# Kernel tuning notes

Measured on AMD Instinct MI355X. Metric: run time of the kernel, lower is better.

The kernel has to match this reference:

```python
import jax, jax.numpy as jnp
import numpy as np

N = 100_000   # nodes
E = 1_600_000 # edges
F = 32        # input features
G = 512       # graphs in batch
EPS = 1e-5    # batchnorm eps


def setup_inputs() -> dict:
    key = jax.random.key(0)
    ks = jax.random.split(key, 24)
    d = {
        "x": jax.random.normal(ks[0], (N, F), jnp.float32),
        "edge_index": jax.random.randint(ks[1], (2, E), 0, N),
        "batch": jnp.sort(jax.random.randint(ks[2], (N,), 0, G)),
        "Wl1": jax.random.normal(ks[3], (30, F), jnp.float32) * 0.1,
        "bl1": jax.random.normal(ks[4], (30,), jnp.float32) * 0.1,
        "Wr1": jax.random.normal(ks[5], (30, F), jnp.float32) * 0.1,
        "Wl2": jax.random.normal(ks[6], (30, 30), jnp.float32) * 0.1,
        "bl2": jax.random.normal(ks[7], (30,), jnp.float32) * 0.1,
        "Wr2": jax.random.normal(ks[8], (30, 30), jnp.float32) * 0.1,
        "g1": jax.random.uniform(ks[9], (30,), jnp.float32) + 0.5,
        "b1": jax.random.normal(ks[10], (30,), jnp.float32) * 0.1,
        "m1": jax.random.normal(ks[11], (30,), jnp.float32) * 0.1,
        "v1": jax.random.uniform(ks[12], (30,), jnp.float32) + 0.5,
        "g2": jax.random.uniform(ks[13], (30,), jnp.float32) + 0.5,
        "b2": jax.random.normal(ks[14], (30,), jnp.float32) * 0.1,
        "m2": jax.random.normal(ks[15], (30,), jnp.float32) * 0.1,
        "v2": jax.random.uniform(ks[16], (30,), jnp.float32) + 0.5,
        "W1": jax.random.normal(ks[17], (10, 60), jnp.float32) * 0.1,
        "bb1": jax.random.normal(ks[18], (10,), jnp.float32) * 0.1,
        "W2": jax.random.normal(ks[19], (1, 10), jnp.float32) * 0.1,
        "bb2": jax.random.normal(ks[20], (1,), jnp.float32) * 0.1,
    }
    return d


def reference(x, edge_index, batch, Wl1, bl1, Wr1, Wl2, bl2, Wr2,
              g1, b1, m1, v1, g2, b2, m2, v2, W1, bb1, W2, bb2):
    src, dst = edge_index[0], edge_index[1]

    def sage(h, Wl, bl, Wr):
        # mean aggregation of source features into targets (PyG SAGEConv default)
        s = jax.ops.segment_sum(h[src], dst, num_segments=N)
        cnt = jax.ops.segment_sum(jnp.ones((E,), h.dtype), dst, num_segments=N)
        agg = s / jnp.maximum(cnt, 1.0)[:, None]
        return agg @ Wl.T + bl + h @ Wr.T

    def bn(h, g, b, m, v):  # BatchNorm1d, eval mode (running stats)
        return (h - m) * jax.lax.rsqrt(v + EPS) * g + b

    h = bn(jax.nn.relu(sage(x, Wl1, bl1, Wr1)), g1, b1, m1, v1)
    h = bn(jax.nn.relu(sage(h, Wl2, bl2, Wr2)), g2, b2, m2, v2)

    # dual segment pooling over graphs
    xmax = jax.ops.segment_max(h, batch, num_segments=G)
    xmax = jnp.where(jnp.isfinite(xmax), xmax, 0.0)  # empty graphs -> 0
    s = jax.ops.segment_sum(h, batch, num_segments=G)
    c = jax.ops.segment_sum(jnp.ones((N,), h.dtype), batch, num_segments=G)
    xmean = s / jnp.maximum(c, 1.0)[:, None]

    z = jnp.concatenate([xmax, xmean], axis=1)  # [G, 60]
    z = jax.nn.relu(z @ W1.T + bb1)
    z = z @ W2.T + bb2
    return jax.nn.sigmoid(z)  # [G, 1]
```

## Files before the change

kernel.cpp:

```cpp
#include <hip/hip_runtime.h>
#include <hip/hip_fp16.h>

#define NN 100000
#define NE 1600000
#define FI 32
#define FH 30
#define PAD 32
#define NG 512
#define NBK 782
#define BNODES 128
#define SCB 2048
#define CBLK 32
#define NCHUNK (SCB / CBLK)
#define CAP 4096
#define NB1 391

__global__ __launch_bounds__(256) void k_phist(const int* __restrict__ dst, int* __restrict__ partial)
{
    __shared__ int cnt[NBK];
    for (int i = threadIdx.x; i < NBK; i += 256) cnt[i] = 0;
    __syncthreads();
    for (int e = blockIdx.x * 256 + threadIdx.x; e < NE; e += SCB * 256)
        atomicAdd(&cnt[dst[e] >> 7], 1);
    __syncthreads();
    for (int i = threadIdx.x; i < NBK; i += 256)
        partial[(size_t)blockIdx.x * NBK + i] = cnt[i];
}

__global__ __launch_bounds__(256) void k_csum(const int* __restrict__ partial, int* __restrict__ chunksum)
{
    int t = blockIdx.x * 256 + threadIdx.x;
    if (t >= NCHUNK * NBK) return;
    int c = t / NBK, b = t - c * NBK;
    int s = 0;
    #pragma unroll 8
    for (int k = 0; k < CBLK; ++k)
        s += partial[(size_t)(c * CBLK + k) * NBK + b];
    chunksum[c * NBK + b] = s;
}

__global__ __launch_bounds__(1024) void k_cscan(const int* __restrict__ chunksum,
                                                int* __restrict__ chunkbase, int* __restrict__ bktOff)
{
    __shared__ int tmp[1024];
    int tid = threadIdx.x;
    int total = 0;
    if (tid < NBK) {
        for (int c = 0; c < NCHUNK; ++c) total += chunksum[c * NBK + tid];
    }
    tmp[tid] = (tid < NBK) ? total : 0;
    __syncthreads();
    for (int off = 1; off < 1024; off <<= 1) {
        int t = (tid >= off) ? tmp[tid - off] : 0;
        __syncthreads();
        tmp[tid] += t;
        __syncthreads();
    }
    if (tid < NBK) {
        int run = tmp[tid] - total;
        bktOff[tid] = run;
        for (int c = 0; c < NCHUNK; ++c) {
            chunkbase[c * NBK + tid] = run;
            run += chunksum[c * NBK + tid];
        }
    }
    if (tid == 0) bktOff[NBK] = NE;
}

__global__ __launch_bounds__(256) void k_base(int* __restrict__ partial, const int* __restrict__ chunkbase)
{
    int t = blockIdx.x * 256 + threadIdx.x;
    if (t >= NCHUNK * NBK) return;
    int c = t / NBK, b = t - c * NBK;
    int run = chunkbase[c * NBK + b];
    #pragma unroll 8
    for (int k = 0; k < CBLK; ++k) {
        size_t idx = (size_t)(c * CBLK + k) * NBK + b;
        int v = partial[idx];
        partial[idx] = run;
        run += v;
    }
}

__global__ __launch_bounds__(256) void k_bscat(const int* __restrict__ src, const int* __restrict__ dst,
                                               const int* __restrict__ partial, unsigned* __restrict__ pairs)
{
    __shared__ int sbase[NBK];
    __shared__ int scnt[NBK];
    for (int i = threadIdx.x; i < NBK; i += 256) {
        sbase[i] = partial[(size_t)blockIdx.x * NBK + i];
        scnt[i] = 0;
    }
    __syncthreads();
    for (int e = blockIdx.x * 256 + threadIdx.x; e < NE; e += SCB * 256) {
        int d = dst[e];
        int b = d >> 7;
        int r = atomicAdd(&scnt[b], 1);
        pairs[sbase[b] + r] = ((unsigned)src[e] << 7) | (unsigned)(d & 127);
    }
}

__global__ __launch_bounds__(256) void k_csr(
    const int* __restrict__ bktOff, const unsigned* __restrict__ pairs,
    int* __restrict__ rowstart, int* __restrict__ col)
{
    __shared__ unsigned sp[CAP];
    __shared__ int bins[BNODES], binpos[BNODES], stmp[BNODES];
    int tid = threadIdx.x;
    int bkt = blockIdx.x;
    int gbase = bktOff[bkt];
    int cnt = bktOff[bkt + 1] - gbase;
    if (tid < BNODES) bins[tid] = 0;
    __syncthreads();
    bool inl = (cnt <= CAP);
    if (inl) {
        for (int i = tid; i < cnt; i += 256) {
            unsigned u = pairs[gbase + i];
            sp[i] = u;
            atomicAdd(&bins[u & 127], 1);
        }
    } else {
        for (int i = tid; i < cnt; i += 256)
            atomicAdd(&bins[pairs[gbase + i] & 127], 1);
    }
    __syncthreads();
    if (tid < BNODES) stmp[tid] = bins[tid];
    __syncthreads();
    for (int off = 1; off < BNODES; off <<= 1) {
        int t = 0;
        if (tid < BNODES && tid >= off) t = stmp[tid - off];
        __syncthreads();
        if (tid < BNODES) stmp[tid] += t;
        __syncthreads();
    }
    if (tid < BNODES) {
        int ex = stmp[tid] - bins[tid];
        binpos[tid] = ex;
        int n = (bkt << 7) + tid;
        if (n < NN) rowstart[n] = gbase + ex;
        if (bkt == 0 && tid == 0) rowstart[NN] = NE;
    }
    __syncthreads();
    if (inl) {
        for (int i = tid; i < cnt; i += 256) {
            unsigned u = sp[i];
            int p = atomicAdd(&binpos[u & 127], 1);
            col[gbase + p] = (int)(u >> 7);
        }
    } else {
        for (int i = tid; i < cnt; i += 256) {
            unsigned u = pairs[gbase + i];
            int p = atomicAdd(&binpos[u & 127], 1);
            col[gbase + p] = (int)(u >> 7);
        }
    }
}

__global__ __launch_bounds__(256) void k_tohalf(const float* __restrict__ in, __half2* __restrict__ outp)
{
    int i = blockIdx.x * 256 + threadIdx.x;
    if (i < NN * (PAD / 2)) {
        float2 f = ((const float2*)in)[i];
        outp[i] = __floats2half2_rn(f.x, f.y);
    }
}

__global__ __launch_bounds__(256) void k_aggcsr_h(const int* __restrict__ rowstart,
                                                  const int* __restrict__ col,
                                                  const uint4* __restrict__ hin,
                                                  float* __restrict__ aggout)
{
    int tid = blockIdx.x * 256 + threadIdx.x;
    int n = tid >> 6;
    if (n >= NN) return;
    int lane = threadIdx.x & 63;
    int q = lane & 3;
    int grp = lane >> 2;
    int rs = rowstart[n], re = rowstart[n + 1];
    float a0 = 0.0f, a1 = 0.0f, a2 = 0.0f, a3 = 0.0f;
    float a4 = 0.0f, a5 = 0.0f, a6 = 0.0f, a7 = 0.0f;
    for (int e = rs + grp; e < re; e += 16) {
        uint4 u = hin[(size_t)col[e] * 4 + q];
        float2 f0 = __half22float2(*(const __half2*)&u.x);
        float2 f1 = __half22float2(*(const __half2*)&u.y);
        float2 f2 = __half22float2(*(const __half2*)&u.z);
        float2 f3 = __half22float2(*(const __half2*)&u.w);
        a0 += f0.x; a1 += f0.y; a2 += f1.x; a3 += f1.y;
        a4 += f2.x; a5 += f2.y; a6 += f3.x; a7 += f3.y;
    }
    #pragma unroll
    for (int off = 4; off < 64; off <<= 1) {
        a0 += __shfl_xor(a0, off); a1 += __shfl_xor(a1, off);
        a2 += __shfl_xor(a2, off); a3 += __shfl_xor(a3, off);
        a4 += __shfl_xor(a4, off); a5 += __shfl_xor(a5, off);
        a6 += __shfl_xor(a6, off); a7 += __shfl_xor(a7, off);
    }
    if (lane < 4) {
        float inv = (re > rs) ? 1.0f / (float)(re - rs) : 0.0f;
        float4* o = (float4*)(aggout + (size_t)n * PAD + q * 8);
        o[0] = make_float4(a0 * inv, a1 * inv, a2 * inv, a3 * inv);
        o[1] = make_float4(a4 * inv, a5 * inv, a6 * inv, a7 * inv);
    }
}

__global__ __launch_bounds__(256) void k_t1(
    const float* __restrict__ x, const float* __restrict__ agg,
    const float* __restrict__ Wl, const float* __restrict__ bl, const float* __restrict__ Wr,
    const float* __restrict__ g, const float* __restrict__ b,
    const float* __restrict__ m, const float* __restrict__ v,
    __half2* __restrict__ h1h)
{
    __shared__ float sWl[FH * FI], sWr[FH * FI], sBias[FH], sScale[FH], sShift[FH];
    for (int i = threadIdx.x; i < FH * FI; i += 256) { sWl[i] = Wl[i]; sWr[i] = Wr[i]; }
    if (threadIdx.x < FH) {
        int j = threadIdx.x;
        float sc = g[j] * rsqrtf(v[j] + 1e-5f);
        sBias[j] = bl[j];
        sScale[j] = sc;
        sShift[j] = b[j] - m[j] * sc;
    }
    __syncthreads();
    int n = blockIdx.x * 256 + threadIdx.x;
    if (n >= NN) return;
    float xr[FI], ar[FI];
    #pragma unroll
    for (int k = 0; k < FI; k += 4) {
        float4 xv = *(const float4*)(x + (size_t)n * FI + k);
        float4 av = *(const float4*)(agg + (size_t)n * PAD + k);
        xr[k] = xv.x; xr[k+1] = xv.y; xr[k+2] = xv.z; xr[k+3] = xv.w;
        ar[k] = av.x; ar[k+1] = av.y; ar[k+2] = av.z; ar[k+3] = av.w;
    }
    float res[FH];
    for (int j = 0; j < FH; ++j) {
        float acc = sBias[j];
        #pragma unroll
        for (int k = 0; k < FI; ++k)
            acc += ar[k] * sWl[j * FI + k] + xr[k] * sWr[j * FI + k];
        acc = fmaxf(acc, 0.0f);
        res[j] = acc * sScale[j] + sShift[j];
    }
    __half2* row = h1h + (size_t)n * (PAD / 2);
    #pragma unroll
    for (int j = 0; j < FH; j += 2)
        row[j >> 1] = __floats2half2_rn(res[j], res[j + 1]);
    row[15] = __floats2half2_rn(0.0f, 0.0f);
}

__global__ __launch_bounds__(256) void k_t2(
    const __half2* __restrict__ h1h, const float* agg,
    const float* __restrict__ Wl, const float* __restrict__ bl, const float* __restrict__ Wr,
    const float* __restrict__ g, const float* __restrict__ b,
    const float* __restrict__ m, const float* __restrict__ v,
    float* hout)
{
    __shared__ float sWl[FH * FH], sWr[FH * FH], sBias[FH], sScale[FH], sShift[FH];
    for (int i = threadIdx.x; i < FH * FH; i += 256) { sWl[i] = Wl[i]; sWr[i] = Wr[i]; }
    if (threadIdx.x < FH) {
        int j = threadIdx.x;
        float sc = g[j] * rsqrtf(v[j] + 1e-5f);
        sBias[j] = bl[j];
        sScale[j] = sc;
        sShift[j] = b[j] - m[j] * sc;
    }
    __syncthreads();
    int n = blockIdx.x * 256 + threadIdx.x;
    if (n >= NN) return;
    float xr[FH], ar[FH];
    const __half2* hrow = h1h + (size_t)n * (PAD / 2);
    #pragma unroll
    for (int k2 = 0; k2 < FH / 2; ++k2) {
        float2 fv = __half22float2(hrow[k2]);
        xr[2 * k2] = fv.x; xr[2 * k2 + 1] = fv.y;
    }
    #pragma unroll
    for (int k = 0; k < FH; ++k)
        ar[k] = agg[(size_t)n * PAD + k];
    float res[FH];
    for (int j = 0; j < FH; ++j) {
        float acc = sBias[j];
        #pragma unroll
        for (int k = 0; k < FH; ++k)
            acc += ar[k] * sWl[j * FH + k] + xr[k] * sWr[j * FH + k];
        acc = fmaxf(acc, 0.0f);
        res[j] = acc * sScale[j] + sShift[j];
    }
    #pragma unroll
    for (int j = 0; j < FH; ++j)
        hout[(size_t)n * PAD + j] = res[j];
}

__global__ __launch_bounds__(256) void k_pool(
    const float* __restrict__ h2, const int* __restrict__ batch,
    const float* __restrict__ W1, const float* __restrict__ bb1,
    const float* __restrict__ W2, const float* __restrict__ bb2,
    float* __restrict__ out)
{
    __shared__ float sS[8][FH], sM[8][FH], sz[2 * FH], st[10];
    int tid = threadIdx.x;
    int gi = blockIdx.x;
    int lo = 0, hi = NN;
    while (lo < hi) { int mid = (lo + hi) >> 1; if (batch[mid] < gi) lo = mid + 1; else hi = mid; }
    int start = lo;
    hi = NN;
    while (lo < hi) { int mid = (lo + hi) >> 1; if (batch[mid] <= gi) lo = mid + 1; else hi = mid; }
    int end = lo;

    int f = tid & 31;
    int ng = tid >> 5;
    float sum = 0.0f, mx = -INFINITY;
    if (f < FH) {
        for (int n = start + ng; n < end; n += 8) {
            float val = h2[(size_t)n * PAD + f];
            sum += val;
            mx = fmaxf(mx, val);
        }
        sS[ng][f] = sum;
        sM[ng][f] = mx;
    }
    __syncthreads();
    if (tid < FH) {
        float s = 0.0f, mm = -INFINITY;
        #pragma unroll
        for (int w = 0; w < 8; ++w) { s += sS[w][tid]; mm = fmaxf(mm, sM[w][tid]); }
        int c = end - start;
        sz[tid]      = (c > 0) ? mm : 0.0f;
        sz[FH + tid] = (c > 0) ? s / (float)c : 0.0f;
    }
    __syncthreads();
    if (tid < 10) {
        float t = bb1[tid];
        for (int k = 0; k < 2 * FH; ++k) t += sz[k] * W1[tid * 2 * FH + k];
        st[tid] = fmaxf(t, 0.0f);
    }
    __syncthreads();
    if (tid == 0) {
        float o = bb2[0];
        for (int j = 0; j < 10; ++j) o += st[j] * W2[j];
        out[gi] = 1.0f / (1.0f + expf(-o));
    }
}

extern "C" void kernel_launch(void* const* d_in, const int* in_sizes, int n_in,
                              void* d_out, int out_size, void* d_ws, size_t ws_size,
                              hipStream_t stream)
{
    const float* x   = (const float*)d_in[0];
    const int*   ei  = (const int*)d_in[1];
    const int*   bat = (const int*)d_in[2];
    const float* Wl1 = (const float*)d_in[3];
    const float* bl1 = (const float*)d_in[4];
    const float* Wr1 = (const float*)d_in[5];
    const float* Wl2 = (const float*)d_in[6];
    const float* bl2 = (const float*)d_in[7];
    const float* Wr2 = (const float*)d_in[8];
    const float* g1  = (const float*)d_in[9];
    const float* b1  = (const float*)d_in[10];
    const float* m1  = (const float*)d_in[11];
    const float* v1  = (const float*)d_in[12];
    const float* g2  = (const float*)d_in[13];
    const float* b2  = (const float*)d_in[14];
    const float* m2  = (const float*)d_in[15];
    const float* v2  = (const float*)d_in[16];
    const float* W1  = (const float*)d_in[17];
    const float* bb1 = (const float*)d_in[18];
    const float* W2  = (const float*)d_in[19];
    const float* bb2 = (const float*)d_in[20];

    const int* src = ei;
    const int* dst = ei + NE;

    int* wsi = (int*)d_ws;
    int*      partial   = wsi;
    int*      chunksum  = partial + (size_t)SCB * NBK;
    int*      chunkbase = chunksum + NCHUNK * NBK;
    int*      bktOff    = chunkbase + NCHUNK * NBK;
    int*      rowstart  = bktOff + NBK + 2;
    unsigned* pairs     = (unsigned*)(rowstart + NN + 4);
    int*      col       = (int*)(pairs + NE);
    __half2*  xh        = (__half2*)(col + NE);
    __half2*  h1h       = xh + (size_t)NN * (PAD / 2);
    float*    aggbuf    = (float*)(h1h + (size_t)NN * (PAD / 2));

    int pb = (NCHUNK * NBK + 255) / 256;

    k_phist <<<SCB, 256, 0, stream>>>(dst, partial);
    k_tohalf<<<(NN * (PAD / 2) + 255) / 256, 256, 0, stream>>>(x, (__half2*)xh);
    k_csum  <<<pb, 256, 0, stream>>>(partial, chunksum);
    k_cscan <<<1, 1024, 0, stream>>>(chunksum, chunkbase, bktOff);
    k_base  <<<pb, 256, 0, stream>>>(partial, chunkbase);
    k_bscat <<<SCB, 256, 0, stream>>>(src, dst, partial, pairs);
    k_csr   <<<NBK, 256, 0, stream>>>(bktOff, pairs, rowstart, col);

    int ab = (NN * 64 + 255) / 256;
    k_aggcsr_h<<<ab, 256, 0, stream>>>(rowstart, col, (const uint4*)xh, aggbuf);
    k_t1<<<NB1, 256, 0, stream>>>(x, aggbuf, Wl1, bl1, Wr1, g1, b1, m1, v1, h1h);
    k_aggcsr_h<<<ab, 256, 0, stream>>>(rowstart, col, (const uint4*)h1h, aggbuf);
    k_t2<<<NB1, 256, 0, stream>>>(h1h, aggbuf, Wl2, bl2, Wr2, g2, b2, m2, v2, aggbuf);
    k_pool<<<NG, 256, 0, stream>>>(aggbuf, bat, W1, bb1, W2, bb2, (float*)d_out);
}
```

Baseline: 202.2 us.

## Fuse neighbor aggregation with SAGE linear, ReLU and batchnorm per layer

Replaces the separate CSR aggregation kernel and per-node transform kernels with one fused kernel per layer. Each wavefront aggregates its node's neighbors, stages the mean and the self features in shared memory, then computes the 30 outputs across lanes and writes fp16. This removes the fp32 aggregate buffer round trip and two launches. The layer-2 output is now stored in fp16 for pooling, and layer 1 uses the fp16 copy of x as self input, which lowers precision. Each of the 25000 blocks also reloads and pads the weight matrices into shared memory.

```diff
diff --git a/kernel.cpp b/kernel.cpp
--- a/kernel.cpp
+++ b/kernel.cpp
@@ -13,7 +13,7 @@
 #define CBLK 32
 #define NCHUNK (SCB / CBLK)
 #define CAP 4096
-#define NB1 391
+#define AB 25000
 
 __global__ __launch_bounds__(256) void k_phist(const int* __restrict__ dst, int* __restrict__ partial)
 {
@@ -165,15 +165,35 @@
     }
 }
 
-__global__ __launch_bounds__(256) void k_aggcsr_h(const int* __restrict__ rowstart,
-                                                  const int* __restrict__ col,
-                                                  const uint4* __restrict__ hin,
-                                                  float* __restrict__ aggout)
-{
-    int tid = blockIdx.x * 256 + threadIdx.x;
-    int n = tid >> 6;
-    if (n >= NN) return;
-    int lane = threadIdx.x & 63;
+__global__ __launch_bounds__(256) void k_fused(
+    const int* __restrict__ rowstart, const int* __restrict__ col,
+    const uint4* __restrict__ hin,
+    const float* __restrict__ Wl, const float* __restrict__ bl, const float* __restrict__ Wr,
+    int K,
+    const float* __restrict__ g, const float* __restrict__ b,
+    const float* __restrict__ m, const float* __restrict__ v,
+    __half2* __restrict__ hout)
+{
+    __shared__ float sWl[FH * 33], sWr[FH * 33];
+    __shared__ float sBias[FH], sScale[FH], sShift[FH];
+    __shared__ float sAgg[4][32], sSelf[4][32];
+    int tid = threadIdx.x;
+    for (int i = tid; i < FH * 32; i += 256) {
+        int j = i >> 5, k = i & 31;
+        sWl[j * 33 + k] = (k < K) ? Wl[j * K + k] : 0.0f;
+        sWr[j * 33 + k] = (k < K) ? Wr[j * K + k] : 0.0f;
+    }
+    if (tid < FH) {
+        float sc = g[tid] * rsqrtf(v[tid] + 1e-5f);
+        sBias[tid] = bl[tid];
+        sScale[tid] = sc;
+        sShift[tid] = b[tid] - m[tid] * sc;
+    }
+    __syncthreads();
+
+    int n = (blockIdx.x * 256 + tid) >> 6;
+    int w = tid >> 6;
+    int lane = tid & 63;
     int q = lane & 3;
     int grp = lane >> 2;
     int rs = rowstart[n], re = rowstart[n + 1];
@@ -197,100 +217,46 @@
     }
     if (lane < 4) {
         float inv = (re > rs) ? 1.0f / (float)(re - rs) : 0.0f;
-        float4* o = (float4*)(aggout + (size_t)n * PAD + q * 8);
-        o[0] = make_float4(a0 * inv, a1 * inv, a2 * inv, a3 * inv);
-        o[1] = make_float4(a4 * inv, a5 * inv, a6 * inv, a7 * inv);
-    }
-}
-
-__global__ __launch_bounds__(256) void k_t1(
-    const float* __restrict__ x, const float* __restrict__ agg,
-    const float* __restrict__ Wl, const float* __restrict__ bl, const float* __restrict__ Wr,
-    const float* __restrict__ g, const float* __restrict__ b,
-    const float* __restrict__ m, const float* __restrict__ v,
-    __half2* __restrict__ h1h)
-{
-    __shared__ float sWl[FH * FI], sWr[FH * FI], sBias[FH], sScale[FH], sShift[FH];
-    for (int i = threadIdx.x; i < FH * FI; i += 256) { sWl[i] = Wl[i]; sWr[i] = Wr[i]; }
-    if (threadIdx.x < FH) {
-        int j = threadIdx.x;
-        float sc = g[j] * rsqrtf(v[j] + 1e-5f);
-        sBias[j] = bl[j];
-        sScale[j] = sc;
-        sShift[j] = b[j] - m[j] * sc;
-    }
-    __syncthreads();
-    int n = blockIdx.x * 256 + threadIdx.x;
-    if (n >= NN) return;
-    float xr[FI], ar[FI];
-    #pragma unroll
-    for (int k = 0; k < FI; k += 4) {
-        float4 xv = *(const float4*)(x + (size_t)n * FI + k);
-        float4 av = *(const float4*)(agg + (size_t)n * PAD + k);
-        xr[k] = xv.x; xr[k+1] = xv.y; xr[k+2] = xv.z; xr[k+3] = xv.w;
-        ar[k] = av.x; ar[k+1] = av.y; ar[k+2] = av.z; ar[k+3] = av.w;
-    }
-    float res[FH];
-    for (int j = 0; j < FH; ++j) {
-        float acc = sBias[j];
+        uint4 su = hin[(size_t)n * 4 + q];
+        float2 s0 = __half22float2(*(const __half2*)&su.x);
+        float2 s1 = __half22float2(*(const __half2*)&su.y);
+        float2 s2 = __half22float2(*(const __half2*)&su.z);
+        float2 s3 = __half22float2(*(const __half2*)&su.w);
+        int base = q * 8;
+        sAgg[w][base + 0] = a0 * inv; sAgg[w][base + 1] = a1 * inv;
+        sAgg[w][base + 2] = a2 * inv; sAgg[w][base + 3] = a3 * inv;
+        sAgg[w][base + 4] = a4 * inv; sAgg[w][base + 5] = a5 * inv;
+        sAgg[w][base + 6] = a6 * inv; sAgg[w][base + 7] = a7 * inv;
+        sSelf[w][base + 0] = s0.x; sSelf[w][base + 1] = s0.y;
+        sSelf[w][base + 2] = s1.x; sSelf[w][base + 3] = s1.y;
+        sSelf[w][base + 4] = s2.x; sSelf[w][base + 5] = s2.y;
+        sSelf[w][base + 6] = s3.x; sSelf[w][base + 7] = s3.y;
+    }
+    __syncthreads();
+
+    int j = lane >> 1;
+    int k0 = (lane & 1) * 16;
+    float partial = 0.0f;
+    if (j < FH) {
         #pragma unroll
-        for (int k = 0; k < FI; ++k)
-            acc += ar[k] * sWl[j * FI + k] + xr[k] * sWr[j * FI + k];
-        acc = fmaxf(acc, 0.0f);
-        res[j] = acc * sScale[j] + sShift[j];
-    }
-    __half2* row = h1h + (size_t)n * (PAD / 2);
-    #pragma unroll
-    for (int j = 0; j < FH; j += 2)
-        row[j >> 1] = __floats2half2_rn(res[j], res[j + 1]);
-    row[15] = __floats2half2_rn(0.0f, 0.0f);
-}
-
-__global__ __launch_bounds__(256) void k_t2(
-    const __half2* __restrict__ h1h, const float* agg,
-    const float* __restrict__ Wl, const float* __restrict__ bl, const float* __restrict__ Wr,
-    const float* __restrict__ g, const float* __restrict__ b,
-    const float* __restrict__ m, const float* __restrict__ v,
-    float* hout)
-{
-    __shared__ float sWl[FH * FH], sWr[FH * FH], sBias[FH], sScale[FH], sShift[FH];
-    for (int i = threadIdx.x; i < FH * FH; i += 256) { sWl[i] = Wl[i]; sWr[i] = Wr[i]; }
-    if (threadIdx.x < FH) {
-        int j = threadIdx.x;
-        float sc = g[j] * rsqrtf(v[j] + 1e-5f);
-        sBias[j] = bl[j];
-        sScale[j] = sc;
-        sShift[j] = b[j] - m[j] * sc;
-    }
-    __syncthreads();
-    int n = blockIdx.x * 256 + threadIdx.x;
-    if (n >= NN) return;
-    float xr[FH], ar[FH];
-    const __half2* hrow = h1h + (size_t)n * (PAD / 2);
-    #pragma unroll
-    for (int k2 = 0; k2 < FH / 2; ++k2) {
-        float2 fv = __half22float2(hrow[k2]);
-        xr[2 * k2] = fv.x; xr[2 * k2 + 1] = fv.y;
-    }
-    #pragma unroll
-    for (int k = 0; k < FH; ++k)
-        ar[k] = agg[(size_t)n * PAD + k];
-    float res[FH];
-    for (int j = 0; j < FH; ++j) {
-        float acc = sBias[j];
-        #pragma unroll
-        for (int k = 0; k < FH; ++k)
-            acc += ar[k] * sWl[j * FH + k] + xr[k] * sWr[j * FH + k];
-        acc = fmaxf(acc, 0.0f);
-        res[j] = acc * sScale[j] + sShift[j];
-    }
-    #pragma unroll
-    for (int j = 0; j < FH; ++j)
-        hout[(size_t)n * PAD + j] = res[j];
+        for (int k = k0; k < k0 + 16; ++k)
+            partial += sAgg[w][k] * sWl[j * 33 + k] + sSelf[w][k] * sWr[j * 33 + k];
+    }
+    partial += __shfl_xor(partial, 1);
+    float res = 0.0f;
+    if (j < FH) {
+        float acc = fmaxf(partial + sBias[j], 0.0f);
+        res = acc * sScale[j] + sShift[j];
+    }
+    int wsel = (lane & 15) * 4;
+    float f0 = __shfl(res, wsel);
+    float f1 = __shfl(res, wsel + 2);
+    if (lane < 16)
+        hout[(size_t)n * 16 + lane] = __floats2half2_rn(f0, f1);
 }
 
 __global__ __launch_bounds__(256) void k_pool(
-    const float* __restrict__ h2, const int* __restrict__ batch,
+    const __half* __restrict__ h2, const int* __restrict__ batch,
     const float* __restrict__ W1, const float* __restrict__ bb1,
     const float* __restrict__ W2, const float* __restrict__ bb2,
     float* __restrict__ out)
@@ -310,7 +276,7 @@
     float sum = 0.0f, mx = -INFINITY;
     if (f < FH) {
         for (int n = start + ng; n < end; n += 8) {
-            float val = h2[(size_t)n * PAD + f];
+            float val = __half2float(h2[(size_t)n * PAD + f]);
             sum += val;
             mx = fmaxf(mx, val);
         }
@@ -379,22 +345,21 @@
     int*      col       = (int*)(pairs + NE);
     __half2*  xh        = (__half2*)(col + NE);
     __half2*  h1h       = xh + (size_t)NN * (PAD / 2);
-    float*    aggbuf    = (float*)(h1h + (size_t)NN * (PAD / 2));
+    __half2*  h2h       = h1h + (size_t)NN * (PAD / 2);
 
     int pb = (NCHUNK * NBK + 255) / 256;
 
     k_phist <<<SCB, 256, 0, stream>>>(dst, partial);
-    k_tohalf<<<(NN * (PAD / 2) + 255) / 256, 256, 0, stream>>>(x, (__half2*)xh);
+    k_tohalf<<<(NN * (PAD / 2) + 255) / 256, 256, 0, stream>>>(x, xh);
     k_csum  <<<pb, 256, 0, stream>>>(partial, chunksum);
     k_cscan <<<1, 1024, 0, stream>>>(chunksum, chunkbase, bktOff);
     k_base  <<<pb, 256, 0, stream>>>(partial, chunkbase);
     k_bscat <<<SCB, 256, 0, stream>>>(src, dst, partial, pairs);
     k_csr   <<<NBK, 256, 0, stream>>>(bktOff, pairs, rowstart, col);
 
-    int ab = (NN * 64 + 255) / 256;
-    k_aggcsr_h<<<ab, 256, 0, stream>>>(rowstart, col, (const uint4*)xh, aggbuf);
-    k_t1<<<NB1, 256, 0, stream>>>(x, aggbuf, Wl1, bl1, Wr1, g1, b1, m1, v1, h1h);
-    k_aggcsr_h<<<ab, 256, 0, stream>>>(rowstart, col, (const uint4*)h1h, aggbuf);
-    k_t2<<<NB1, 256, 0, stream>>>(h1h, aggbuf, Wl2, bl2, Wr2, g2, b2, m2, v2, aggbuf);
-    k_pool<<<NG, 256, 0, stream>>>(aggbuf, bat, W1, bb1, W2, bb2, (float*)d_out);
-}
+    k_fused<<<AB, 256, 0, stream>>>(rowstart, col, (const uint4*)xh,
+                                    Wl1, bl1, Wr1, FI, g1, b1, m1, v1, h1h);
+    k_fused<<<AB, 256, 0, stream>>>(rowstart, col, (const uint4*)h1h,
+                                    Wl2, bl2, Wr2, FH, g2, b2, m2, v2, h2h);
+    k_pool<<<NG, 256, 0, stream>>>((const __half*)h2h, bat, W1, bb1, W2, bb2, (float*)d_out);
+}
```

New measurement: 245.5 us. +21.4%, slower.
